# Kernel optimization log

Measured on AMD Instinct MI355X. Metric: run time of the kernel, lower is better.

## Reference

```python
import jax, jax.numpy as jnp
import numpy as np

CHANNELS = 128
HEADS = 4
R = 2
LAMBDA = 0.1


def setup_inputs() -> dict:
    key = jax.random.key(0)
    k1, k2 = jax.random.split(key)
    x = jax.random.normal(k1, (1, CHANNELS, 32, 32, 32), dtype=jnp.float32)
    # 1x1x1 Conv3d weight [3C, C] (trailing unit spatial dims dropped), fan-in scaled
    w_qkv = jax.random.normal(k2, (3 * CHANNELS, CHANNELS), dtype=jnp.float32) * (CHANNELS ** -0.5)
    return {"x": x, "w_qkv": w_qkv}


def reference(x, w_qkv):
    head_dim = CHANNELS // HEADS          # 32
    d_half = head_dim // 2                # 16
    scale = head_dim ** -0.5
    # AvgPool3d(kernel_size=1, stride=R) == strided subsampling
    xs = x[:, :, ::R, ::R, ::R]
    B, C, H, W, Z = xs.shape
    N = H * W * Z                          # 4096 tokens
    # 1x1x1 conv == pointwise channel matmul, then group channels heads-major
    qkv = jnp.einsum('oc,bchwz->bohwz', w_qkv, xs).reshape(B, HEADS, 3 * head_dim, N)
    q, k, v = jnp.split(qkv, 3, axis=2)    # each [B, h, head_dim, N]
    q1, q2 = q[:, :, :d_half, :], q[:, :, d_half:, :]
    k1, k2 = k[:, :, :d_half, :], k[:, :, d_half:, :]
    # two full score matrices [B, h, N, N] (differential attention)
    attn1 = jnp.einsum('bhdn,bhdm->bhnm', q1, k1) * scale
    attn2 = jnp.einsum('bhdn,bhdm->bhnm', q2, k2) * scale
    diff_attn = jax.nn.softmax(attn1, axis=-1) - LAMBDA * jax.nn.softmax(attn2, axis=-1)
    out = jnp.einsum('bhnm,bhdm->bhnd', diff_attn, v)  # [B, h, N, head_dim]
    # faithful to torch .view(B, -1, H, W, Z) on contiguous (h, N, head_dim) layout
    return out.reshape(B, C, H, W, Z)
```

## Files before the change

### kernel.cpp

```cpp
#include <hip/hip_runtime.h>

#define N_TOK 4096
#define NH    4

typedef __attribute__((ext_vector_type(8))) short bf16x8;
typedef __attribute__((ext_vector_type(4))) short bf16x4;
typedef __attribute__((ext_vector_type(4))) float f32x4;

static constexpr float SCALE   = 0.17677669529663687f;
static constexpr float QSCALE  = 0.25503632254435463f;
static constexpr float LAMBDA_ = 0.1f;
#define PSTRIDE 2112

__device__ __forceinline__ unsigned short bf_rne(float f) {
    unsigned u = __float_as_uint(f);
    u += 0x7FFF + ((u >> 16) & 1);
    return (unsigned short)(u >> 16);
}

__device__ __forceinline__ void async_copy16(const unsigned short* g, unsigned short* l) {
    __builtin_amdgcn_global_load_lds(
        (const __attribute__((address_space(1))) void*)g,
        (__attribute__((address_space(3))) void*)l, 16, 0, 0);
}

__global__ __launch_bounds__(512) void qkv_kernel(
    const float* __restrict__ x, const float* __restrict__ w,
    unsigned short* __restrict__ qA, unsigned short* __restrict__ kB,
    unsigned short* __restrict__ vT)
{
    __shared__ __align__(16) float w_sh[384][18];
    __shared__ __align__(16) float xst[16][132];
    __shared__ __align__(16) unsigned short qsh[4][16][64];
    __shared__ __align__(16) unsigned short ksh[4][16][64];
    __shared__ __align__(16) unsigned short vsh[4][32][16];

    const int t  = threadIdx.x;
    const int n0 = blockIdx.x * 16;
    const int nh = n0 >> 8, nw = (n0 >> 4) & 15;
    const int xbase = nh * 2048 + nw * 64;

    #pragma unroll
    for (int k = 0; k < 4; ++k) {
        int idx = t + k * 512;
        int tok = idx & 15, ch = idx >> 4;
        xst[tok][ch] = x[(size_t)ch * 32768 + xbase + tok * 2];
    }

    float acc[3][4];
    #pragma unroll
    for (int k = 0; k < 3; ++k)
        #pragma unroll
        for (int j = 0; j < 4; ++j) acc[k][j] = 0.f;

    for (int chunk = 0; chunk < 8; ++chunk) {
        __syncthreads();
        #pragma unroll
        for (int k = 0; k < 3; ++k) {
            int idx = t + k * 512;
            int row = idx >> 2, c4 = idx & 3;
            float4 wv = *(const float4*)(w + (size_t)row * 128 + chunk * 16 + c4 * 4);
            *(float2*)&w_sh[row][c4 * 4]     = make_float2(wv.x, wv.y);
            *(float2*)&w_sh[row][c4 * 4 + 2] = make_float2(wv.z, wv.w);
        }
        __syncthreads();
        #pragma unroll
        for (int k = 0; k < 3; ++k) {
            int u = t + k * 512;
            int row = u >> 2, quad = u & 3;
            #pragma unroll
            for (int c16 = 0; c16 < 4; ++c16) {
                float2 wa = *(const float2*)&w_sh[row][c16 * 4];
                float2 wb = *(const float2*)&w_sh[row][c16 * 4 + 2];
                #pragma unroll
                for (int j = 0; j < 4; ++j) {
                    float4 xv = *(const float4*)&xst[quad * 4 + j][chunk * 16 + c16 * 4];
                    acc[k][j] += wa.x * xv.x + wa.y * xv.y + wb.x * xv.z + wb.y * xv.w;
                }
            }
        }
    }

    #pragma unroll
    for (int k = 0; k < 3; ++k) {
        int u = t + k * 512;
        int row = u >> 2, quad = u & 3;
        int hh = row / 96, r = row - hh * 96;
        if (r < 64) {
            int rr = r & 31, part = rr >> 4, d = rr & 15;
            float sc = (r < 32) ? QSCALE : 1.0f;
            #pragma unroll
            for (int j = 0; j < 4; ++j) {
                int tok = quad * 4 + j;
                float f = acc[k][j] * sc;
                unsigned u32 = __float_as_uint(f);
                float lo = f - __uint_as_float(u32 & 0xFFFF0000u);
                unsigned short hi16 = (unsigned short)(u32 >> 16);
                unsigned short lo16 = (unsigned short)(__float_as_uint(lo) >> 16);
                if (r < 32) {
                    qsh[hh][tok][part * 32 + d]      = hi16;
                    qsh[hh][tok][part * 32 + d + 16] = lo16;
                } else {
                    ksh[hh][tok][part * 32 + d]      = hi16;
                    ksh[hh][tok][part * 32 + d + 16] = lo16;
                }
            }
        } else {
            int d = r - 64;
            #pragma unroll
            for (int j = 0; j < 4; ++j)
                vsh[hh][d][quad * 4 + j] = bf_rne(acc[k][j]);
        }
    }
    __syncthreads();
    {
        int rec = t >> 3, ch8 = t & 7;
        int hh  = rec >> 4, i = rec & 15;
        size_t base = ((size_t)hh * N_TOK + n0 + i) * 64 + ch8 * 8;
        *(uint4*)(qA + base) = *(const uint4*)&qsh[hh][i][ch8 * 8];
        *(uint4*)(kB + base) = *(const uint4*)&ksh[hh][i][ch8 * 8];
    }
    if (t < 256) {
        int hh = t >> 6, d = (t >> 1) & 31, half = t & 1;
        int kb = (n0 >> 3) + half;
        *(uint4*)(vT + (size_t)hh * 131072 + kb * 256 + d * 8) =
            *(const uint4*)&vsh[hh][d][half * 8];
    }
}

__global__ __launch_bounds__(256, 4) void flash_kernel(
    const unsigned short* __restrict__ qA, const unsigned short* __restrict__ kB,
    const unsigned short* __restrict__ vT, float* __restrict__ parts)
{
    __shared__ __align__(16) unsigned short kv_sh[2][6144];
    __shared__ float Obuf[2][2][16][32];
    __shared__ float lbuf[2][2][16];

    const int t    = threadIdx.x;
    const int w    = t >> 6;
    const int lane = t & 63;
    const int m    = lane & 15;
    const int quad = lane >> 4;
    const int ks   = blockIdx.x & 1;
    const int qt   = (blockIdx.x >> 1) & 127;
    const int h    = blockIdx.x >> 8;
    const int qtile = w >> 1;
    const int kh    = w & 1;
    const int qbase = qt * 32;

    const unsigned short* kBh = kB + (size_t)h * N_TOK * 64;
    const unsigned short* vTh = vT + (size_t)h * 131072;
    const int key0 = ks * 2048;

    auto stage = [&](int tile, int b) {
        const unsigned short* kben = kBh + (size_t)(key0 + tile * 64) * 64;
        const unsigned short* vben = vTh + (size_t)((key0 >> 3) + tile * 8) * 256;
        #pragma unroll
        for (int i = 0; i < 3; ++i) {
            int s = i * 256 + t;
            const unsigned short* src;
            if (s < 512) {
                int ml = s >> 3, p = s & 7, c = p ^ (ml & 7);
                src = kben + ml * 64 + c * 8;
            } else {
                int s2 = s - 512;
                int kb_l = s2 >> 5, d = s2 & 31;
                src = vben + kb_l * 256 + d * 8;
            }
            async_copy16(src, &kv_sh[b][s * 8]);
        }
    };

    stage(0, 0);

    for (int i = t; i < 2048; i += 256) ((float*)Obuf)[i] = 0.f;
    if (t < 64) ((float*)lbuf)[t] = 0.f;

    const unsigned short* qrec = qA + (size_t)(h * N_TOK + qbase + qtile * 16 + m) * 64;
    const bf16x8 zz = {0,0,0,0,0,0,0,0};
    bf16x8 Bq1h = *(const bf16x8*)(qrec + (quad & 1) * 8);
    bf16x8 Bq2h = *(const bf16x8*)(qrec + 32 + (quad & 1) * 8);
    bf16x8 Bq1l = (quad < 2) ? *(const bf16x8*)(qrec + 16 + quad * 8) : zz;
    bf16x8 Bq2l = (quad < 2) ? *(const bf16x8*)(qrec + 48 + quad * 8) : zz;

    f32x4 O1a = {0,0,0,0}, O1b = {0,0,0,0}, O2a = {0,0,0,0}, O2b = {0,0,0,0};
    float l1 = 0.f, l2 = 0.f;

    const int ml0 = kh * 32 + m, ml1 = ml0 + 16;
    const int a1o0 = ml0 * 64 + ((quad)     ^ (ml0 & 7)) * 8;
    const int a2o0 = ml0 * 64 + ((4 + quad) ^ (ml0 & 7)) * 8;
    const int a1o1 = ml1 * 64 + ((quad)     ^ (ml1 & 7)) * 8;
    const int a2o1 = ml1 * 64 + ((4 + quad) ^ (ml1 & 7)) * 8;
    const int kbl0 = kh * 4 + (quad >> 1);
    const int v0o0 = 4096 + (kbl0 * 32 + m)      * 8 + (quad & 1) * 4;
    const int v1o0 = 4096 + (kbl0 * 32 + 16 + m) * 8 + (quad & 1) * 4;
    const int v0o1 = v0o0 + 512;
    const int v1o1 = v1o0 + 512;

    for (int tile = 0; tile < 32; ++tile) {
        const int b = tile & 1;
        __syncthreads();
        if (tile + 1 < 32) stage(tile + 1, b ^ 1);

        const unsigned short* buf = kv_sh[b];
        bf16x8 K1_0 = *(const bf16x8*)(buf + a1o0);
        bf16x8 K2_0 = *(const bf16x8*)(buf + a2o0);
        bf16x8 K1_1 = *(const bf16x8*)(buf + a1o1);
        bf16x8 K2_1 = *(const bf16x8*)(buf + a2o1);

        f32x4 sA1 = {0,0,0,0}, sA2 = {0,0,0,0};
        f32x4 sB1 = {0,0,0,0}, sB2 = {0,0,0,0};
        sA1 = __builtin_amdgcn_mfma_f32_16x16x32_bf16(K1_0, Bq1h, sA1, 0, 0, 0);
        sB1 = __builtin_amdgcn_mfma_f32_16x16x32_bf16(K1_1, Bq1h, sB1, 0, 0, 0);
        sA1 = __builtin_amdgcn_mfma_f32_16x16x32_bf16(K1_0, Bq1l, sA1, 0, 0, 0);
        sB1 = __builtin_amdgcn_mfma_f32_16x16x32_bf16(K1_1, Bq1l, sB1, 0, 0, 0);
        sA2 = __builtin_amdgcn_mfma_f32_16x16x32_bf16(K2_0, Bq2h, sA2, 0, 0, 0);
        sB2 = __builtin_amdgcn_mfma_f32_16x16x32_bf16(K2_1, Bq2h, sB2, 0, 0, 0);
        sA2 = __builtin_amdgcn_mfma_f32_16x16x32_bf16(K2_0, Bq2l, sA2, 0, 0, 0);
        sB2 = __builtin_amdgcn_mfma_f32_16x16x32_bf16(K2_1, Bq2l, sB2, 0, 0, 0);

        float pa0 = __builtin_amdgcn_exp2f(sA1[0]), pa1 = __builtin_amdgcn_exp2f(sA1[1]);
        float pa2 = __builtin_amdgcn_exp2f(sA1[2]), pa3 = __builtin_amdgcn_exp2f(sA1[3]);
        float pb0 = __builtin_amdgcn_exp2f(sB1[0]), pb1 = __builtin_amdgcn_exp2f(sB1[1]);
        float pb2 = __builtin_amdgcn_exp2f(sB1[2]), pb3 = __builtin_amdgcn_exp2f(sB1[3]);
        float qa0 = __builtin_amdgcn_exp2f(sA2[0]), qa1 = __builtin_amdgcn_exp2f(sA2[1]);
        float qa2 = __builtin_amdgcn_exp2f(sA2[2]), qa3 = __builtin_amdgcn_exp2f(sA2[3]);
        float qb0 = __builtin_amdgcn_exp2f(sB2[0]), qb1 = __builtin_amdgcn_exp2f(sB2[1]);
        float qb2 = __builtin_amdgcn_exp2f(sB2[2]), qb3 = __builtin_amdgcn_exp2f(sB2[3]);
        l1 += (pa0 + pa1) + (pa2 + pa3) + (pb0 + pb1) + (pb2 + pb3);
        l2 += (qa0 + qa1) + (qa2 + qa3) + (qb0 + qb1) + (qb2 + qb3);
        union { unsigned u[2]; bf16x4 v; } cA1, cB1, cA2, cB2;
        cA1.u[0] = __builtin_amdgcn_perm(__float_as_uint(pa1), __float_as_uint(pa0), 0x07060302u);
        cA1.u[1] = __builtin_amdgcn_perm(__float_as_uint(pa3), __float_as_uint(pa2), 0x07060302u);
        cB1.u[0] = __builtin_amdgcn_perm(__float_as_uint(pb1), __float_as_uint(pb0), 0x07060302u);
        cB1.u[1] = __builtin_amdgcn_perm(__float_as_uint(pb3), __float_as_uint(pb2), 0x07060302u);
        cA2.u[0] = __builtin_amdgcn_perm(__float_as_uint(qa1), __float_as_uint(qa0), 0x07060302u);
        cA2.u[1] = __builtin_amdgcn_perm(__float_as_uint(qa3), __float_as_uint(qa2), 0x07060302u);
        cB2.u[0] = __builtin_amdgcn_perm(__float_as_uint(qb1), __float_as_uint(qb0), 0x07060302u);
        cB2.u[1] = __builtin_amdgcn_perm(__float_as_uint(qb3), __float_as_uint(qb2), 0x07060302u);

        bf16x4 V00 = *(const bf16x4*)(buf + v0o0);
        bf16x4 V10 = *(const bf16x4*)(buf + v1o0);
        bf16x4 V01 = *(const bf16x4*)(buf + v0o1);
        bf16x4 V11 = *(const bf16x4*)(buf + v1o1);

        O1a = __builtin_amdgcn_mfma_f32_16x16x16bf16_1k(cA1.v, V00, O1a, 0, 0, 0);
        O1b = __builtin_amdgcn_mfma_f32_16x16x16bf16_1k(cA1.v, V10, O1b, 0, 0, 0);
        O2a = __builtin_amdgcn_mfma_f32_16x16x16bf16_1k(cA2.v, V00, O2a, 0, 0, 0);
        O2b = __builtin_amdgcn_mfma_f32_16x16x16bf16_1k(cA2.v, V10, O2b, 0, 0, 0);
        O1a = __builtin_amdgcn_mfma_f32_16x16x16bf16_1k(cB1.v, V01, O1a, 0, 0, 0);
        O1b = __builtin_amdgcn_mfma_f32_16x16x16bf16_1k(cB1.v, V11, O1b, 0, 0, 0);
        O2a = __builtin_amdgcn_mfma_f32_16x16x16bf16_1k(cB2.v, V01, O2a, 0, 0, 0);
        O2b = __builtin_amdgcn_mfma_f32_16x16x16bf16_1k(cB2.v, V11, O2b, 0, 0, 0);
    }

    l1 += __shfl_xor(l1, 16, 64); l1 += __shfl_xor(l1, 32, 64);
    l2 += __shfl_xor(l2, 16, 64); l2 += __shfl_xor(l2, 32, 64);
    if (lane < 16) {
        atomicAdd(&lbuf[qtile][0][m], l1);
        atomicAdd(&lbuf[qtile][1][m], l2);
    }
    #pragma unroll
    for (int i = 0; i < 4; ++i) {
        int r = quad * 4 + i;
        atomicAdd(&Obuf[qtile][0][r][m],      O1a[i]);
        atomicAdd(&Obuf[qtile][0][r][16 + m], O1b[i]);
        atomicAdd(&Obuf[qtile][1][r][m],      O2a[i]);
        atomicAdd(&Obuf[qtile][1][r][16 + m], O2b[i]);
    }
    __syncthreads();

    float* dst = parts + (size_t)((h * 128 + qt) * 2 + ks) * PSTRIDE;
    for (int i = t; i < 1024; i += 256) {
        int r = i >> 5, d = i & 31;
        int qtl = r >> 4, rl = r & 15;
        dst[i]        = Obuf[qtl][0][rl][d];
        dst[1024 + i] = Obuf[qtl][1][rl][d];
    }
    if (t < 32) {
        int qtl = t >> 4, rl = t & 15;
        dst[2048 + t] = lbuf[qtl][0][rl];
        dst[2080 + t] = lbuf[qtl][1][rl];
    }
}

__global__ __launch_bounds__(256) void merge_kernel(
    const float* __restrict__ parts, float* __restrict__ out)
{
    int idx = blockIdx.x * 256 + threadIdx.x;
    int row = idx >> 5, d = idx & 31;
    int h = row >> 12, n = row & 4095;
    int qt = n >> 5, r = n & 31;
    const float* p0 = parts + (size_t)((h * 128 + qt) * 2) * PSTRIDE;
    const float* p1 = p0 + PSTRIDE;
    float o1 = p0[r * 32 + d]        + p1[r * 32 + d];
    float o2 = p0[1024 + r * 32 + d] + p1[1024 + r * 32 + d];
    float l1 = p0[2048 + r]          + p1[2048 + r];
    float l2 = p0[2080 + r]          + p1[2080 + r];
    out[idx] = o1 / l1 - LAMBDA_ * o2 / l2;
}

extern "C" void kernel_launch(void* const* d_in, const int* in_sizes, int n_in,
                              void* d_out, int out_size, void* d_ws, size_t ws_size,
                              hipStream_t stream) {
    const float* x = (const float*)d_in[0];
    const float* w = (const float*)d_in[1];
    float* out = (float*)d_out;

    unsigned short* qA = (unsigned short*)d_ws;
    unsigned short* kB = qA + (size_t)NH * N_TOK * 64;
    unsigned short* vT = kB + (size_t)NH * N_TOK * 64;
    float* parts = (float*)(vT + (size_t)NH * 32 * N_TOK);

    qkv_kernel<<<256, 512, 0, stream>>>(x, w, qA, kB, vT);
    flash_kernel<<<1024, 256, 0, stream>>>(qA, kB, vT, parts);
    merge_kernel<<<2048, 256, 0, stream>>>(parts, out);
}
```

Before: 144.1 us.

## Compute QKV projection with split-bf16 MFMA and a weight pre-split kernel

The scalar FP32 QKV projection is replaced with bf16 MFMA using a hi/lo split (three MFMAs per step) so it stays close to FP32 accuracy. A new prep kernel pre-scales the weights and splits them into bf16 hi/lo arrays in workspace. The QKV grid doubles to 512 blocks of 256 threads, with each block covering half the output rows. This adds one kernel launch and extra workspace traffic in exchange for matrix-core throughput. The QKV stage is likely a small part of total time next to the flash kernel.

After: 134.2 us. 1.07x faster.

```diff
diff --git a/kernel.cpp b/kernel.cpp
--- a/kernel.cpp
+++ b/kernel.cpp
@@ -24,107 +24,131 @@
         (__attribute__((address_space(3))) void*)l, 16, 0, 0);
 }
 
-__global__ __launch_bounds__(512) void qkv_kernel(
-    const float* __restrict__ x, const float* __restrict__ w,
+__global__ __launch_bounds__(256) void prep_w_kernel(
+    const float* __restrict__ w,
+    unsigned short* __restrict__ wh, unsigned short* __restrict__ wl)
+{
+    int idx = blockIdx.x * 256 + threadIdx.x;
+    int row = idx >> 7;
+    int rr  = row % 96;
+    float sc = (rr < 32) ? QSCALE : 1.0f;
+    float f  = w[idx] * sc;
+    unsigned u = __float_as_uint(f);
+    float lo = f - __uint_as_float(u & 0xFFFF0000u);
+    wh[idx] = (unsigned short)(u >> 16);
+    wl[idx] = (unsigned short)(__float_as_uint(lo) >> 16);
+}
+
+__global__ __launch_bounds__(256) void qkv_kernel(
+    const float* __restrict__ x,
+    const unsigned short* __restrict__ wh, const unsigned short* __restrict__ wl,
     unsigned short* __restrict__ qA, unsigned short* __restrict__ kB,
     unsigned short* __restrict__ vT)
 {
-    __shared__ __align__(16) float w_sh[384][18];
-    __shared__ __align__(16) float xst[16][132];
-    __shared__ __align__(16) unsigned short qsh[4][16][64];
-    __shared__ __align__(16) unsigned short ksh[4][16][64];
-    __shared__ __align__(16) unsigned short vsh[4][32][16];
+    __shared__ __align__(16) float xf[16][132];
+    __shared__ __align__(16) unsigned short xbh[16 * 136];
+    __shared__ __align__(16) unsigned short xbl[16 * 136];
+    __shared__ __align__(16) unsigned short qsh[2][16][64];
+    __shared__ __align__(16) unsigned short ksh[2][16][64];
+    __shared__ __align__(16) unsigned short vsh[2][32][16];
 
     const int t  = threadIdx.x;
-    const int n0 = blockIdx.x * 16;
+    const int tg = blockIdx.x >> 1;
+    const int rh = blockIdx.x & 1;
+    const int n0 = tg * 16;
     const int nh = n0 >> 8, nw = (n0 >> 4) & 15;
     const int xbase = nh * 2048 + nw * 64;
 
     #pragma unroll
-    for (int k = 0; k < 4; ++k) {
-        int idx = t + k * 512;
+    for (int k = 0; k < 8; ++k) {
+        int idx = t + k * 256;
         int tok = idx & 15, ch = idx >> 4;
-        xst[tok][ch] = x[(size_t)ch * 32768 + xbase + tok * 2];
-    }
-
-    float acc[3][4];
-    #pragma unroll
-    for (int k = 0; k < 3; ++k)
+        xf[tok][ch] = x[(size_t)ch * 32768 + xbase + tok * 2];
+    }
+    __syncthreads();
+    #pragma unroll
+    for (int k = 0; k < 8; ++k) {
+        int idx = t + k * 256;
+        int tok = idx & 15, ch = idx >> 4;
+        float f = xf[tok][ch];
+        unsigned u = __float_as_uint(f);
+        float lo = f - __uint_as_float(u & 0xFFFF0000u);
+        xbh[tok * 136 + ch] = (unsigned short)(u >> 16);
+        xbl[tok * 136 + ch] = (unsigned short)(__float_as_uint(lo) >> 16);
+    }
+    __syncthreads();
+
+    const int lane = t & 63;
+    const int m    = lane & 15;
+    const int quad = lane >> 4;
+    const int w    = t >> 6;
+
+    bf16x8 Bh[4], Bl[4];
+    #pragma unroll
+    for (int s = 0; s < 4; ++s) {
+        Bh[s] = *(const bf16x8*)&xbh[m * 136 + s * 32 + quad * 8];
+        Bl[s] = *(const bf16x8*)&xbl[m * 136 + s * 32 + quad * 8];
+    }
+
+    #pragma unroll
+    for (int rt = 0; rt < 3; ++rt) {
+        const int R0 = rh * 192 + w * 48 + rt * 16;
+        const unsigned short* whp = wh + (size_t)(R0 + m) * 128;
+        const unsigned short* wlp = wl + (size_t)(R0 + m) * 128;
+        bf16x8 Ah[4], Al[4];
         #pragma unroll
-        for (int j = 0; j < 4; ++j) acc[k][j] = 0.f;
-
-    for (int chunk = 0; chunk < 8; ++chunk) {
-        __syncthreads();
+        for (int s = 0; s < 4; ++s) {
+            Ah[s] = *(const bf16x8*)(whp + s * 32 + quad * 8);
+            Al[s] = *(const bf16x8*)(wlp + s * 32 + quad * 8);
+        }
+        f32x4 C = {0, 0, 0, 0};
         #pragma unroll
-        for (int k = 0; k < 3; ++k) {
-            int idx = t + k * 512;
-            int row = idx >> 2, c4 = idx & 3;
-            float4 wv = *(const float4*)(w + (size_t)row * 128 + chunk * 16 + c4 * 4);
-            *(float2*)&w_sh[row][c4 * 4]     = make_float2(wv.x, wv.y);
-            *(float2*)&w_sh[row][c4 * 4 + 2] = make_float2(wv.z, wv.w);
+        for (int s = 0; s < 4; ++s) {
+            C = __builtin_amdgcn_mfma_f32_16x16x32_bf16(Ah[s], Bh[s], C, 0, 0, 0);
+            C = __builtin_amdgcn_mfma_f32_16x16x32_bf16(Al[s], Bh[s], C, 0, 0, 0);
+            C = __builtin_amdgcn_mfma_f32_16x16x32_bf16(Ah[s], Bl[s], C, 0, 0, 0);
         }
-        __syncthreads();
         #pragma unroll
-        for (int k = 0; k < 3; ++k) {
-            int u = t + k * 512;
-            int row = u >> 2, quad = u & 3;
-            #pragma unroll
-            for (int c16 = 0; c16 < 4; ++c16) {
-                float2 wa = *(const float2*)&w_sh[row][c16 * 4];
-                float2 wb = *(const float2*)&w_sh[row][c16 * 4 + 2];
-                #pragma unroll
-                for (int j = 0; j < 4; ++j) {
-                    float4 xv = *(const float4*)&xst[quad * 4 + j][chunk * 16 + c16 * 4];
-                    acc[k][j] += wa.x * xv.x + wa.y * xv.y + wb.x * xv.z + wb.y * xv.w;
+        for (int i = 0; i < 4; ++i) {
+            int R  = R0 + quad * 4 + i;
+            int hh = R / 96;
+            int rr = R - hh * 96;
+            int hl = hh & 1;
+            float f = C[i];
+            if (rr < 64) {
+                unsigned u = __float_as_uint(f);
+                float lo = f - __uint_as_float(u & 0xFFFF0000u);
+                unsigned short hi16 = (unsigned short)(u >> 16);
+                unsigned short lo16 = (unsigned short)(__float_as_uint(lo) >> 16);
+                int part = (rr & 31) >> 4, d = rr & 15;
+                if (rr < 32) {
+                    qsh[hl][m][part * 32 + d]      = hi16;
+                    qsh[hl][m][part * 32 + d + 16] = lo16;
+                } else {
+                    ksh[hl][m][part * 32 + d]      = hi16;
+                    ksh[hl][m][part * 32 + d + 16] = lo16;
                 }
+            } else {
+                vsh[hl][rr - 64][m] = bf_rne(f);
             }
         }
     }
-
-    #pragma unroll
-    for (int k = 0; k < 3; ++k) {
-        int u = t + k * 512;
-        int row = u >> 2, quad = u & 3;
-        int hh = row / 96, r = row - hh * 96;
-        if (r < 64) {
-            int rr = r & 31, part = rr >> 4, d = rr & 15;
-            float sc = (r < 32) ? QSCALE : 1.0f;
-            #pragma unroll
-            for (int j = 0; j < 4; ++j) {
-                int tok = quad * 4 + j;
-                float f = acc[k][j] * sc;
-                unsigned u32 = __float_as_uint(f);
-                float lo = f - __uint_as_float(u32 & 0xFFFF0000u);
-                unsigned short hi16 = (unsigned short)(u32 >> 16);
-                unsigned short lo16 = (unsigned short)(__float_as_uint(lo) >> 16);
-                if (r < 32) {
-                    qsh[hh][tok][part * 32 + d]      = hi16;
-                    qsh[hh][tok][part * 32 + d + 16] = lo16;
-                } else {
-                    ksh[hh][tok][part * 32 + d]      = hi16;
-                    ksh[hh][tok][part * 32 + d + 16] = lo16;
-                }
-            }
-        } else {
-            int d = r - 64;
-            #pragma unroll
-            for (int j = 0; j < 4; ++j)
-                vsh[hh][d][quad * 4 + j] = bf_rne(acc[k][j]);
-        }
-    }
     __syncthreads();
+
     {
         int rec = t >> 3, ch8 = t & 7;
-        int hh  = rec >> 4, i = rec & 15;
+        int hl  = rec >> 4, i = rec & 15;
+        int hh  = rh * 2 + hl;
         size_t base = ((size_t)hh * N_TOK + n0 + i) * 64 + ch8 * 8;
-        *(uint4*)(qA + base) = *(const uint4*)&qsh[hh][i][ch8 * 8];
-        *(uint4*)(kB + base) = *(const uint4*)&ksh[hh][i][ch8 * 8];
-    }
-    if (t < 256) {
-        int hh = t >> 6, d = (t >> 1) & 31, half = t & 1;
+        *(uint4*)(qA + base) = *(const uint4*)&qsh[hl][i][ch8 * 8];
+        *(uint4*)(kB + base) = *(const uint4*)&ksh[hl][i][ch8 * 8];
+    }
+    if (t < 128) {
+        int hl = t >> 6, d = (t >> 1) & 31, half = t & 1;
+        int hh = rh * 2 + hl;
         int kb = (n0 >> 3) + half;
         *(uint4*)(vT + (size_t)hh * 131072 + kb * 256 + d * 8) =
-            *(const uint4*)&vsh[hh][d][half * 8];
+            *(const uint4*)&vsh[hl][d][half * 8];
     }
 }
 
@@ -311,8 +335,11 @@
     unsigned short* kB = qA + (size_t)NH * N_TOK * 64;
     unsigned short* vT = kB + (size_t)NH * N_TOK * 64;
     float* parts = (float*)(vT + (size_t)NH * 32 * N_TOK);
-
-    qkv_kernel<<<256, 512, 0, stream>>>(x, w, qA, kB, vT);
+    unsigned short* wh = (unsigned short*)(parts + (size_t)1024 * PSTRIDE);
+    unsigned short* wl = wh + 384 * 128;
+
+    prep_w_kernel<<<192, 256, 0, stream>>>(w, wh, wl);
+    qkv_kernel<<<512, 256, 0, stream>>>(x, wh, wl, qA, kB, vT);
     flash_kernel<<<1024, 256, 0, stream>>>(qA, kB, vT, parts);
     merge_kernel<<<2048, 256, 0, stream>>>(parts, out);
 }
```
